# Kernel tuning notes

Measured on AMD Instinct MI355X. Metric: run time of the kernel, lower is better.

## Reference

```python
import jax, jax.numpy as jnp
import numpy as np
from jax import lax

B, C, H, W = 16, 128, 64, 64
S = 16  # d_state


def setup_inputs() -> dict:
    key = jax.random.key(0)
    ks = jax.random.split(key, 12)
    d = {
        'x': jax.random.normal(ks[0], (B, C, H, W), jnp.float32),
        'conv_w': jax.random.normal(ks[1], (C, C, 3, 3), jnp.float32) * (1.0 / np.sqrt(C * 9)),
        'conv_b': jax.random.normal(ks[2], (C,), jnp.float32) * 0.01,
        'dt_w': jax.random.normal(ks[3], (C, C), jnp.float32) * (1.0 / np.sqrt(C)),
        'dt_b': jax.random.normal(ks[4], (C,), jnp.float32) * 0.01,
        'A': jax.random.normal(ks[5], (C, S), jnp.float32),
        'D': jax.random.normal(ks[6], (C,), jnp.float32),
        'g1_w': jax.random.normal(ks[7], (C, C), jnp.float32) * (1.0 / np.sqrt(C)),
        'g1_b': jax.random.normal(ks[8], (C,), jnp.float32) * 0.01,
        'g2_w': jax.random.normal(ks[9], (C, C), jnp.float32) * (1.0 / np.sqrt(C)),
        'g2_b': jax.random.normal(ks[10], (C,), jnp.float32) * 0.01,
    }
    return d


def _forward(x, conv_w, conv_b, dt_w, dt_b, A, D, g1_w, g1_b, g2_w, g2_b):
    identity = x
    # 3x3 conv, padding=1 (SAME)
    x = lax.conv_general_dilated(x, conv_w, (1, 1), 'SAME',
                                 dimension_numbers=('NCHW', 'OIHW', 'NCHW'))
    x = x + conv_b[None, :, None, None]
    # spectral gate: global avg pool -> 1x1 conv -> relu -> 1x1 conv -> sigmoid
    pooled = jnp.mean(x, axis=(2, 3))                       # [B, C]
    g = jax.nn.relu(jnp.einsum('bc,oc->bo', pooled, g1_w) + g1_b)
    g = jax.nn.sigmoid(jnp.einsum('bc,oc->bo', g, g2_w) + g2_b)
    x = x * g[:, :, None, None]
    # ssm scan over H*W tokens
    x_seq = x.transpose(0, 2, 3, 1).reshape(x.shape[0], H * W, C)  # [B, L, C]
    dt = jax.nn.sigmoid(jnp.einsum('blc,oc->blo', x_seq, dt_w) + dt_b)
    An = -jnp.exp(A)   # [C, S]
    Dp = jnp.exp(D)    # [C]

    def step(h, inp):
        xt, dtt = inp  # each [B, C]
        h = h * jnp.exp(An[None] * dtt[:, :, None]) + xt[:, :, None]  # [B, C, S]
        y = jnp.sum(h * An[None], axis=-1) + Dp * xt                   # [B, C]
        return h, y

    h0 = jnp.zeros((x.shape[0], C, S), x.dtype)
    xs = (x_seq.transpose(1, 0, 2), dt.transpose(1, 0, 2))  # [L, B, C]
    _, ys = lax.scan(step, h0, xs)                           # ys: [L, B, C]
    y = ys.transpose(1, 0, 2).reshape(x.shape[0], H, W, C).transpose(0, 3, 1, 2)
    return y + identity


def reference(x, conv_w, conv_b, dt_w, dt_b, A, D, g1_w, g1_b, g2_w, g2_b):
    return _forward(x, conv_w, conv_b, dt_w, dt_b, A, D, g1_w, g1_b, g2_w, g2_b)
```

## Files before the change

### kernel.cpp

```cpp
#include <hip/hip_runtime.h>
#include <hip/hip_bf16.h>
#include <stdint.h>

#define BB 16
#define CC 128
#define HH 64
#define WW 64
#define LL 4096
#define SS 16
#define NCH 64
#define CT 64

typedef __attribute__((ext_vector_type(2))) float f32x2;
typedef __attribute__((ext_vector_type(4))) float f32x4;
typedef __attribute__((ext_vector_type(8))) short short8;
typedef __attribute__((ext_vector_type(4))) unsigned int u32x4;

#define AS1 __attribute__((address_space(1)))
#define AS3 __attribute__((address_space(3)))

__device__ __forceinline__ float bf2f(unsigned short u) {
    union { unsigned int i; float f; } v;
    v.i = ((unsigned int)u) << 16;
    return v.f;
}
__device__ __forceinline__ float asf(unsigned int u) {
    union { unsigned int i; float f; } v;
    v.i = u;
    return v.f;
}
__device__ __forceinline__ unsigned short f2bf(float f) {
    union { float f; unsigned int i; } v;
    v.f = f;
    unsigned int x = v.i;
    return (unsigned short)((x + 0x7fffu + ((x >> 16) & 1u)) >> 16);
}
__device__ __forceinline__ float fexp2(float x) { return __builtin_amdgcn_exp2f(x); }

__global__ __launch_bounds__(256) void k0(const float* __restrict__ x, unsigned short* __restrict__ xT,
                                          const float* __restrict__ conv_w, const float* __restrict__ dt_w,
                                          const float* __restrict__ A, const float* __restrict__ Dv,
                                          const float* __restrict__ g1w, const float* __restrict__ g2w,
                                          short* __restrict__ wf, short* __restrict__ wdtf,
                                          float* __restrict__ An, float* __restrict__ An2, float* __restrict__ Dp,
                                          float* __restrict__ pooled, float* __restrict__ g1wT, float* __restrict__ g2wT) {
    __shared__ float lt[64][65];
    int bid = blockIdx.x;
    int tid = threadIdx.x;
    if (bid < 2048) {
        int b = bid >> 7, rem = bid & 127;
        int tt = rem >> 1, ct = rem & 1;
        int t0 = tt * 64, c0 = ct * 64;
        int colr = tid & 63, rowb = tid >> 6;
#pragma unroll
        for (int r = 0; r < 16; ++r) {
            int row = rowb + r * 4;
            lt[row][colr] = x[(size_t)(b * CC + c0 + row) * LL + t0 + colr];
        }
        __syncthreads();
#pragma unroll
        for (int r = 0; r < 16; ++r) {
            int trow = rowb + r * 4;
            xT[((size_t)b * LL + t0 + trow) * CC + c0 + colr] = f2bf(lt[colr][trow]);
        }
        return;
    }
    int idx = (bid - 2048) * 256 + tid;
    if (idx < 18432) {
        int lane = idx & 63, fr = idx >> 6;
        int nfg = fr & 7, ks = (fr >> 3) & 3, tp = fr >> 5;
        int dy = tp / 3, dx = tp % 3;
        int cout = nfg * 16 + (lane & 15);
        int cin0 = ks * 32 + (lane >> 4) * 8;
        short8 v;
#pragma unroll
        for (int j = 0; j < 8; ++j)
            v[j] = (short)f2bf(conv_w[((cout * CC + cin0 + j) * 3 + dy) * 3 + dx]);
        *(short8*)(wf + (size_t)idx * 8) = v;
    } else if (idx < 20480) {
        int i2 = idx - 18432;
        int lane = i2 & 63, fr = i2 >> 6;
        int nfg = fr & 7, ks = fr >> 3;
        int o = nfg * 16 + (lane & 15);
        int c0 = ks * 32 + (lane >> 4) * 8;
        short8 v;
#pragma unroll
        for (int j = 0; j < 8; ++j) v[j] = (short)f2bf(dt_w[o * CC + c0 + j]);
        *(short8*)(wdtf + (size_t)i2 * 8) = v;
    } else if (idx < 22528) {
        int i3 = idx - 20480;
        float a = -expf(A[i3]);
        An[i3] = a;
        An2[i3] = a * 1.4426950408889634f;
    } else if (idx < 22656) {
        int c = idx - 22528;
        Dp[c] = expf(Dv[c]);
    } else if (idx < 24704) {
        pooled[idx - 22656] = 0.f;
    } else if (idx < 41088) {
        int i = idx - 24704;
        int c = i >> 7, o = i & 127;
        g1wT[i] = g1w[o * 128 + c];
    } else if (idx < 57472) {
        int i = idx - 41088;
        int c = i >> 7, o = i & 127;
        g2wT[i] = g2w[o * 128 + c];
    }
}

__global__ __launch_bounds__(256) void k1(const unsigned short* __restrict__ xT,
                                          const short* __restrict__ wf,
                                          const float* __restrict__ conv_b,
                                          unsigned short* __restrict__ convT,
                                          float* __restrict__ pooled) {
    __shared__ __align__(16) unsigned short slab[3 * 66 * 128];
    int bid = blockIdx.x;
    int b = bid >> 6, h = bid & 63;
    int tid = threadIdx.x;
    int wave = tid >> 6, lane = tid & 63;

    if (tid < 96) {
        int dy = tid >> 5, r = (tid >> 4) & 1, j = tid & 15;
        u32x4 z = {0, 0, 0, 0};
        *(u32x4*)((char*)slab + dy * 16896 + (r ? 16640 : 0) + j * 16) = z;
    }
#pragma unroll
    for (int dy = 0; dy < 3; ++dy) {
        int hs = h + dy - 1;
        char* slabdy = (char*)slab + dy * 16896;
        if (hs >= 0 && hs < HH) {
            const char* src = (const char*)xT + (size_t)(b * LL + hs * 64) * 256;
#pragma unroll
            for (int i = 0; i < 4; ++i) {
                unsigned int Xbase = 256u + (unsigned)i * 4096u + (unsigned)wave * 1024u;
                unsigned int X = Xbase + (unsigned)lane * 16u;
                unsigned int tok = X >> 8;
                unsigned int srcoff = ((X & ~255u) - 256u) | ((X & 255u) ^ ((tok & 7u) << 4));
                __builtin_amdgcn_global_load_lds((const AS1 unsigned int*)(src + srcoff),
                                                 (AS3 unsigned int*)(slabdy + Xbase), 16, 0, 0);
            }
        } else {
            u32x4 z = {0, 0, 0, 0};
#pragma unroll
            for (int i = 0; i < 4; ++i)
                *(u32x4*)(slabdy + 256 + tid * 64 + i * 16) = z;
        }
    }
    __syncthreads();

    int lm = lane & 15, lg = lane >> 4;
    f32x4 acc[4][2];
#pragma unroll
    for (int m = 0; m < 4; ++m)
#pragma unroll
        for (int n = 0; n < 2; ++n) acc[m][n] = (f32x4){0.f, 0.f, 0.f, 0.f};

#pragma unroll
    for (int tp = 0; tp < 9; ++tp) {
        int dy = tp / 3, dx = tp % 3;
        const char* slabdy = (const char*)slab + dy * 16896;
#pragma unroll
        for (int ks = 0; ks < 4; ++ks) {
            short8 bf0 = *(const short8*)(wf + ((size_t)(((tp * 4 + ks) * 8) + wave * 2 + 0) * 64 + lane) * 8);
            short8 bf1 = *(const short8*)(wf + ((size_t)(((tp * 4 + ks) * 8) + wave * 2 + 1) * 64 + lane) * 8);
#pragma unroll
            for (int mf = 0; mf < 4; ++mf) {
                int tok = mf * 16 + lm + dx;
                unsigned int off = (unsigned)((tok * 256 + ks * 64 + lg * 16) ^ ((tok & 7) << 4));
                short8 af = *(const short8*)(slabdy + off);
                acc[mf][0] = __builtin_amdgcn_mfma_f32_16x16x32_bf16(af, bf0, acc[mf][0], 0, 0, 0);
                acc[mf][1] = __builtin_amdgcn_mfma_f32_16x16x32_bf16(af, bf1, acc[mf][1], 0, 0, 0);
            }
        }
    }

    int n0w = wave * 32;
    size_t tokbase = (size_t)(b * LL + h * 64);
    float psum[2] = {0.f, 0.f};
#pragma unroll
    for (int nf = 0; nf < 2; ++nf) {
        int n = n0w + nf * 16 + lm;
        float bias = conv_b[n];
#pragma unroll
        for (int mf = 0; mf < 4; ++mf)
#pragma unroll
            for (int r = 0; r < 4; ++r) {
                int w = mf * 16 + lg * 4 + r;
                float v = acc[mf][nf][r] + bias;
                convT[(tokbase + w) * CC + n] = f2bf(v);
                psum[nf] += v;
            }
    }
#pragma unroll
    for (int nf = 0; nf < 2; ++nf) {
        float s = psum[nf];
        s += __shfl_xor(s, 16);
        s += __shfl_xor(s, 32);
        if (lane < 16) atomicAdd(&pooled[b * CC + n0w + nf * 16 + lane], s);
    }
}

__global__ __launch_bounds__(128) void k2(const float* __restrict__ pooled,
                                          const float* __restrict__ g1wT, const float* __restrict__ g1b,
                                          const float* __restrict__ g2wT, const float* __restrict__ g2b,
                                          float* __restrict__ gate) {
    __shared__ float meanr[128];
    __shared__ float garr[128];
    int b = blockIdx.x;
    int tid = threadIdx.x;
    meanr[tid] = pooled[b * CC + tid] * (1.f / 4096.f);
    __syncthreads();
    float acc = g1b[tid];
    for (int c = 0; c < 128; ++c) acc += meanr[c] * g1wT[c * 128 + tid];
    garr[tid] = fmaxf(acc, 0.f);
    __syncthreads();
    float acc2 = g2b[tid];
    for (int c = 0; c < 128; ++c) acc2 += garr[c] * g2wT[c * 128 + tid];
    gate[b * CC + tid] = __builtin_amdgcn_rcpf(1.f + fexp2(-1.4426950408889634f * acc2));
}

__global__ __launch_bounds__(256) void k3(const unsigned short* __restrict__ convT,
                                          const short* __restrict__ wdtf,
                                          const float* __restrict__ gate,
                                          const float* __restrict__ dt_b,
                                          const float* __restrict__ An2,
                                          unsigned short* __restrict__ dtT,
                                          unsigned int* __restrict__ xdt,
                                          float* __restrict__ hend, float* __restrict__ decay,
                                          int packed) {
    __shared__ __align__(16) unsigned short albuf[64 * 128];
    __shared__ __align__(16) unsigned short dtl[64 * 136];
    __shared__ float gl[128];
    int bid = blockIdx.x;
    int b = bid >> 6, ch = bid & 63, t0 = ch * 64;
    int tid = threadIdx.x;
    int wave = tid >> 6, lane = tid & 63;

    if (tid < 128) gl[tid] = gate[b * CC + tid];
    __syncthreads();

    const char* srcb = (const char*)convT + (size_t)(b * LL + t0) * 256;
#pragma unroll
    for (int i = 0; i < 4; ++i) {
        unsigned int byteoff = (unsigned)((i * 256 + tid) * 16);
        unsigned int tok = byteoff >> 8;
        unsigned int inner = byteoff & 255u;
        int c8 = (int)(inner >> 1);
        short8 v = *(const short8*)(srcb + (size_t)tok * 256 + inner);
#pragma unroll
        for (int j = 0; j < 8; ++j) {
            float f = bf2f((unsigned short)v[j]) * gl[c8 + j];
            v[j] = (short)f2bf(f);
        }
        *(short8*)((char*)albuf + (byteoff ^ ((tok & 7u) << 4))) = v;
    }
    __syncthreads();

    int lm = lane & 15, lg = lane >> 4;
    f32x4 acc[4][2];
#pragma unroll
    for (int m = 0; m < 4; ++m)
#pragma unroll
        for (int n = 0; n < 2; ++n) acc[m][n] = (f32x4){0.f, 0.f, 0.f, 0.f};
#pragma unroll
    for (int ks = 0; ks < 4; ++ks) {
        short8 bf0 = *(const short8*)(wdtf + ((size_t)((ks * 8) + wave * 2 + 0) * 64 + lane) * 8);
        short8 bf1 = *(const short8*)(wdtf + ((size_t)((ks * 8) + wave * 2 + 1) * 64 + lane) * 8);
#pragma unroll
        for (int mf = 0; mf < 4; ++mf) {
            int tok = mf * 16 + lm;
            unsigned int off = (unsigned)((tok * 256 + ks * 64 + lg * 16) ^ ((tok & 7) << 4));
            short8 af = *(const short8*)((const char*)albuf + off);
            acc[mf][0] = __builtin_amdgcn_mfma_f32_16x16x32_bf16(af, bf0, acc[mf][0], 0, 0, 0);
            acc[mf][1] = __builtin_amdgcn_mfma_f32_16x16x32_bf16(af, bf1, acc[mf][1], 0, 0, 0);
        }
    }
#pragma unroll
    for (int nf = 0; nf < 2; ++nf) {
        int o = wave * 32 + nf * 16 + lm;
        float zb = dt_b[o];
#pragma unroll
        for (int mf = 0; mf < 4; ++mf)
#pragma unroll
            for (int r = 0; r < 4; ++r) {
                int tok = mf * 16 + lg * 4 + r;
                float z = acc[mf][nf][r] + zb;
                float d = __builtin_amdgcn_rcpf(1.f + fexp2(-1.4426950408889634f * z));
                unsigned short ub = f2bf(d);
                if (!packed) dtT[(size_t)(b * LL + t0 + tok) * CC + o] = ub;
                dtl[tok * 136 + o] = ub;
            }
    }
    __syncthreads();

    if (packed) {
        int c = tid & 127, tq2 = tid >> 7;
        unsigned int* xdrow = xdt + ((size_t)b * CC + c) * LL + t0 + tq2 * 32;
#pragma unroll
        for (int k = 0; k < 8; ++k) {
            u32x4 w4;
#pragma unroll
            for (int j = 0; j < 4; ++j) {
                int t = tq2 * 32 + k * 4 + j;
                unsigned int xoff = ((unsigned)(t * 256 + c * 2)) ^ (((unsigned)t & 7u) << 4);
                unsigned short xu = *(const unsigned short*)((const char*)albuf + xoff);
                unsigned short du = dtl[t * 136 + c];
                w4[j] = (((unsigned int)du) << 16) | (unsigned int)xu;
            }
            *(u32x4*)(xdrow + k * 4) = w4;
        }
    }

    int c = tid & 127, shalf = tid >> 7, s0 = shalf * 8;
    float a2[8], h[8];
#pragma unroll
    for (int q = 0; q < 2; ++q) {
        f32x4 av = *(const f32x4*)(An2 + c * SS + s0 + q * 4);
#pragma unroll
        for (int j = 0; j < 4; ++j) { a2[q * 4 + j] = av[j]; h[q * 4 + j] = 0.f; }
    }
    float sdt = 0.f;
#pragma unroll 4
    for (int t = 0; t < CT; ++t) {
        unsigned int xoff = ((unsigned)(t * 256 + c * 2)) ^ (((unsigned)t & 7u) << 4);
        float x = bf2f(*(const unsigned short*)((const char*)albuf + xoff));
        float d = bf2f(dtl[t * 136 + c]);
        sdt += d;
#pragma unroll
        for (int s = 0; s < 8; ++s) h[s] = h[s] * fexp2(a2[s] * d) + x;
    }
    size_t base = ((size_t)(b * NCH + ch) * CC + c) * SS + s0;
#pragma unroll
    for (int q = 0; q < 2; ++q) {
        f32x4 hv, dv;
#pragma unroll
        for (int j = 0; j < 4; ++j) {
            hv[j] = h[q * 4 + j];
            dv[j] = fexp2(a2[q * 4 + j] * sdt);
        }
        *(f32x4*)(hend + base + q * 4) = hv;
        *(f32x4*)(decay + base + q * 4) = dv;
    }
}

__global__ __launch_bounds__(256) void k5(const float* __restrict__ hend, const float* __restrict__ decay,
                                          float* __restrict__ H0) {
    int idx = blockIdx.x * 256 + threadIdx.x;
    int b = idx >> 11, rem = idx & 2047;
    size_t base = (size_t)(b * NCH) * 2048 + rem;
    float Hv = 0.f;
    float he = hend[base], de = decay[base];
#pragma unroll 4
    for (int k = 0; k < NCH - 1; ++k) {
        size_t nbase = base + 2048;
        float hn = hend[nbase];
        float dn = decay[nbase];
        H0[base] = Hv;
        Hv = he + Hv * de;
        he = hn; de = dn; base = nbase;
    }
    H0[base] = Hv;
}

__global__ __launch_bounds__(256, 4) void k6p(const unsigned int* __restrict__ xdt,
                                              const float* __restrict__ Antab,
                                              const float* __restrict__ An2tab,
                                              const float* __restrict__ Dp,
                                              const float* __restrict__ H0,
                                              const float* __restrict__ xin,
                                              float* __restrict__ out) {
    __shared__ unsigned short ylds[128][66];
    int bid = blockIdx.x;
    int b = bid >> 6, ch = bid & 63;
    int tid = threadIdx.x;
    int wave = tid >> 6, lane = tid & 63;
    int t0 = ch * CT;
    int c = wave * 32 + (lane & 31);
    int shalf = lane >> 5;
    int s0 = shalf * 8;

    f32x2 a22[4], anv[4], h2[4];
#pragma unroll
    for (int q = 0; q < 2; ++q) {
        f32x4 av = *(const f32x4*)(An2tab + c * SS + s0 + q * 4);
        f32x4 nv = *(const f32x4*)(Antab + c * SS + s0 + q * 4);
        a22[q * 2 + 0] = (f32x2){av[0], av[1]};
        a22[q * 2 + 1] = (f32x2){av[2], av[3]};
        anv[q * 2 + 0] = (f32x2){nv[0], nv[1]};
        anv[q * 2 + 1] = (f32x2){nv[2], nv[3]};
    }
    size_t hbase = ((size_t)(b * NCH + ch) * CC + c) * SS + s0;
#pragma unroll
    for (int q = 0; q < 2; ++q) {
        f32x4 hv = *(const f32x4*)(H0 + hbase + q * 4);
        h2[q * 2 + 0] = (f32x2){hv[0], hv[1]};
        h2[q * 2 + 1] = (f32x2){hv[2], hv[3]};
    }
    float dpc = (shalf == 0) ? Dp[c] : 0.f;
    const u32x4* xdp = (const u32x4*)(xdt + ((size_t)b * CC + c) * LL + t0);

#pragma unroll 4
    for (int t4 = 0; t4 < 16; ++t4) {
        u32x4 w4 = xdp[t4];
#pragma unroll
        for (int j = 0; j < 4; ++j) {
            unsigned int w = w4[j];
            float x = asf(w << 16);
            float d = asf(w & 0xffff0000u);
            f32x2 x2 = {x, x};
            f32x2 d2 = {d, d};
            f32x2 y2 = {0.f, 0.f};
#pragma unroll
            for (int q = 0; q < 4; ++q) {
                f32x2 tq = a22[q] * d2;
                f32x2 e2;
                e2.x = fexp2(tq.x);
                e2.y = fexp2(tq.y);
                h2[q] = h2[q] * e2 + x2;
                y2 += h2[q] * anv[q];
            }
            float yp = y2.x + y2.y + dpc * x;
            float yo = yp + __shfl_xor(yp, 32);
            if (shalf == 0) ylds[c][t4 * 4 + j] = f2bf(yo);
        }
    }
    __syncthreads();

    int tq = tid & 15, rbase = tid >> 4;
#pragma unroll
    for (int k = 0; k < 8; ++k) {
        int row = k * 16 + rbase;
        size_t gi = (size_t)(b * CC + row) * LL + t0 + tq * 4;
        f32x4 xi = *(const f32x4*)(xin + gi);
        f32x4 yo;
#pragma unroll
        for (int j = 0; j < 4; ++j) yo[j] = bf2f(ylds[row][tq * 4 + j]) + xi[j];
        *(f32x4*)(out + gi) = yo;
    }
}

__global__ __launch_bounds__(256, 4) void k6f(const unsigned short* __restrict__ convT,
                                              const unsigned short* __restrict__ dtT,
                                              const float* __restrict__ gate,
                                              const float* __restrict__ Antab,
                                              const float* __restrict__ An2tab,
                                              const float* __restrict__ Dp,
                                              const float* __restrict__ H0,
                                              const float* __restrict__ xin,
                                              float* __restrict__ out) {
    __shared__ unsigned short ylds[128][66];
    int bid = blockIdx.x;
    int b = bid >> 6, ch = bid & 63;
    int tid = threadIdx.x;
    int wave = tid >> 6, lane = tid & 63;
    int t0 = ch * CT;
    int c = wave * 32 + (lane & 31);
    int shalf = lane >> 5;
    int s0 = shalf * 8;

    float a2[8], an[8], h[8];
#pragma unroll
    for (int q = 0; q < 2; ++q) {
        f32x4 av = *(const f32x4*)(An2tab + c * SS + s0 + q * 4);
        f32x4 nv = *(const f32x4*)(Antab + c * SS + s0 + q * 4);
#pragma unroll
        for (int j = 0; j < 4; ++j) { a2[q * 4 + j] = av[j]; an[q * 4 + j] = nv[j]; }
    }
    size_t hbase = ((size_t)(b * NCH + ch) * CC + c) * SS + s0;
#pragma unroll
    for (int q = 0; q < 2; ++q) {
        f32x4 hv = *(const f32x4*)(H0 + hbase + q * 4);
#pragma unroll
        for (int j = 0; j < 4; ++j) h[q * 4 + j] = hv[j];
    }
    float g = gate[b * CC + c];
    float dpc = (shalf == 0) ? Dp[c] : 0.f;
    const unsigned short* xp = convT + (size_t)(b * LL + t0) * CC + c;
    const unsigned short* dp = dtT + (size_t)(b * LL + t0) * CC + c;

#pragma unroll 4
    for (int t = 0; t < CT; ++t) {
        float x = bf2f(xp[t * CC]) * g;
        float d = bf2f(dp[t * CC]);
        float y0 = dpc * x, y1 = 0.f;
#pragma unroll
        for (int s = 0; s < 8; ++s) {
            h[s] = h[s] * fexp2(a2[s] * d) + x;
            if (s & 1) y1 += h[s] * an[s]; else y0 += h[s] * an[s];
        }
        float yp = y0 + y1;
        float yo = yp + __shfl_xor(yp, 32);
        if (shalf == 0) ylds[c][t] = f2bf(yo);
    }
    __syncthreads();

    int tt = tid & 63, wq = tid >> 6;
    size_t outbase = (size_t)b * CC * LL + t0 + tt;
#pragma unroll 4
    for (int rr = 0; rr < 32; ++rr) {
        int row = rr * 4 + wq;
        size_t gi = outbase + (size_t)row * LL;
        out[gi] = bf2f(ylds[row][tt]) + xin[gi];
    }
}

extern "C" void kernel_launch(void* const* d_in, const int* in_sizes, int n_in,
                              void* d_out, int out_size, void* d_ws, size_t ws_size,
                              hipStream_t stream) {
    const float* x      = (const float*)d_in[0];
    const float* conv_w = (const float*)d_in[1];
    const float* conv_b = (const float*)d_in[2];
    const float* dt_w   = (const float*)d_in[3];
    const float* dt_b   = (const float*)d_in[4];
    const float* A      = (const float*)d_in[5];
    const float* D      = (const float*)d_in[6];
    const float* g1w    = (const float*)d_in[7];
    const float* g1b    = (const float*)d_in[8];
    const float* g2w    = (const float*)d_in[9];
    const float* g2b    = (const float*)d_in[10];
    float* outp         = (float*)d_out;
    char* ws = (char*)d_ws;

    const bool P = (ws_size >= 67600896ull);

    unsigned short* xT;
    float *hend, *decay, *H0, *g1wT, *g2wT, *pooled, *gate, *Antab, *An2tab, *Dp;
    unsigned short *convT, *dtT;
    unsigned int* xdt;
    short *wf, *wdtf;

    if (P) {
        xT     = (unsigned short*)(ws + 0);
        hend   = (float*)(ws + 0);
        decay  = (float*)(ws + 8388608);
        convT  = (unsigned short*)(ws + 16777216);
        H0     = (float*)(ws + 16777216);
        xdt    = (unsigned int*)(ws + 33554432);
        dtT    = (unsigned short*)(ws + 33554432);
        wf     = (short*)(ws + 67108864);
        wdtf   = (short*)(ws + 67403776);
        pooled = (float*)(ws + 67436544);
        gate   = (float*)(ws + 67444736);
        Antab  = (float*)(ws + 67452928);
        An2tab = (float*)(ws + 67461120);
        Dp     = (float*)(ws + 67469312);
        g1wT   = (float*)(ws + 67469824);
        g2wT   = (float*)(ws + 67535360);
    } else {
        xT     = (unsigned short*)(ws + 0);
        hend   = (float*)(ws + 0);
        decay  = (float*)(ws + 8388608);
        convT  = (unsigned short*)(ws + 16777216);
        dtT    = (unsigned short*)(ws + 33554432);
        xdt    = (unsigned int*)(ws + 33554432);
        H0     = (float*)(ws + 50331648);
        g1wT   = (float*)(ws + 50331648);
        g2wT   = (float*)(ws + 50397184);
        wf     = (short*)(ws + 58720256);
        wdtf   = (short*)(ws + 59015168);
        pooled = (float*)(ws + 59047936);
        gate   = (float*)(ws + 59056128);
        Antab  = (float*)(ws + 59064320);
        An2tab = (float*)(ws + 59072512);
        Dp     = (float*)(ws + 59080704);
    }

    hipLaunchKernelGGL(k0, dim3(2273), dim3(256), 0, stream, x, xT, conv_w, dt_w, A, D, g1w, g2w,
                       wf, wdtf, Antab, An2tab, Dp, pooled, g1wT, g2wT);
    hipLaunchKernelGGL(k1, dim3(1024), dim3(256), 0, stream, xT, wf, conv_b, convT, pooled);
    hipLaunchKernelGGL(k2, dim3(16), dim3(128), 0, stream, pooled, g1wT, g1b, g2wT, g2b, gate);
    hipLaunchKernelGGL(k3, dim3(1024), dim3(256), 0, stream, convT, wdtf, gate, dt_b, An2tab,
                       dtT, xdt, hend, decay, (int)P);
    hipLaunchKernelGGL(k5, dim3(128), dim3(256), 0, stream, hend, decay, H0);
    if (P) {
        hipLaunchKernelGGL(k6p, dim3(1024), dim3(256), 0, stream, (const unsigned int*)xdt,
                           Antab, An2tab, Dp, H0, x, outp);
    } else {
        hipLaunchKernelGGL(k6f, dim3(1024), dim3(256), 0, stream, convT, dtT, gate,
                           Antab, An2tab, Dp, H0, x, outp);
    }
}
```

Baseline: 126.8 us.

## Split k6p across channel halves with 4 states per lane and quad reductions

The final scan-apply kernel now processes half the channels per block across twice as many blocks. Each lane holds 4 state entries instead of 8, and the per-token output is reduced with two xor shuffles across lane quads. Launch bounds are raised to 6 blocks per CU. The packed writer in k3 is remapped so 16 lanes cover consecutive tokens of one channel, making the global stores more contiguous. The intent is better parallelism and occupancy in the serial scan, at the cost of an extra shuffle per token and more redundant exp work per value loaded.

New measurement: 129.6 us. 1.02x slower.

```diff
diff --git a/kernel.cpp b/kernel.cpp
--- a/kernel.cpp
+++ b/kernel.cpp
@@ -294,20 +294,21 @@
     __syncthreads();
 
     if (packed) {
-        int c = tid & 127, tq2 = tid >> 7;
-        unsigned int* xdrow = xdt + ((size_t)b * CC + c) * LL + t0 + tq2 * 32;
+        int tquad = tid & 15;
+        int cb = tid >> 4;
 #pragma unroll
         for (int k = 0; k < 8; ++k) {
+            int c = k * 16 + cb;
             u32x4 w4;
 #pragma unroll
             for (int j = 0; j < 4; ++j) {
-                int t = tq2 * 32 + k * 4 + j;
+                int t = tquad * 4 + j;
                 unsigned int xoff = ((unsigned)(t * 256 + c * 2)) ^ (((unsigned)t & 7u) << 4);
                 unsigned short xu = *(const unsigned short*)((const char*)albuf + xoff);
                 unsigned short du = dtl[t * 136 + c];
                 w4[j] = (((unsigned int)du) << 16) | (unsigned int)xu;
             }
-            *(u32x4*)(xdrow + k * 4) = w4;
+            *(u32x4*)(xdt + ((size_t)b * CC + c) * LL + t0 + tquad * 4) = w4;
         }
     }
 
@@ -362,41 +363,34 @@
     H0[base] = Hv;
 }
 
-__global__ __launch_bounds__(256, 4) void k6p(const unsigned int* __restrict__ xdt,
+__global__ __launch_bounds__(256, 6) void k6p(const unsigned int* __restrict__ xdt,
                                               const float* __restrict__ Antab,
                                               const float* __restrict__ An2tab,
                                               const float* __restrict__ Dp,
                                               const float* __restrict__ H0,
                                               const float* __restrict__ xin,
                                               float* __restrict__ out) {
-    __shared__ unsigned short ylds[128][66];
+    __shared__ unsigned short ylds[64][66];
     int bid = blockIdx.x;
-    int b = bid >> 6, ch = bid & 63;
+    int b = bid >> 7, rem = bid & 127;
+    int ch = rem >> 1, chalf = rem & 1;
     int tid = threadIdx.x;
     int wave = tid >> 6, lane = tid & 63;
     int t0 = ch * CT;
-    int c = wave * 32 + (lane & 31);
-    int shalf = lane >> 5;
-    int s0 = shalf * 8;
-
-    f32x2 a22[4], anv[4], h2[4];
-#pragma unroll
-    for (int q = 0; q < 2; ++q) {
-        f32x4 av = *(const f32x4*)(An2tab + c * SS + s0 + q * 4);
-        f32x4 nv = *(const f32x4*)(Antab + c * SS + s0 + q * 4);
-        a22[q * 2 + 0] = (f32x2){av[0], av[1]};
-        a22[q * 2 + 1] = (f32x2){av[2], av[3]};
-        anv[q * 2 + 0] = (f32x2){nv[0], nv[1]};
-        anv[q * 2 + 1] = (f32x2){nv[2], nv[3]};
-    }
-    size_t hbase = ((size_t)(b * NCH + ch) * CC + c) * SS + s0;
-#pragma unroll
-    for (int q = 0; q < 2; ++q) {
-        f32x4 hv = *(const f32x4*)(H0 + hbase + q * 4);
-        h2[q * 2 + 0] = (f32x2){hv[0], hv[1]};
-        h2[q * 2 + 1] = (f32x2){hv[2], hv[3]};
-    }
-    float dpc = (shalf == 0) ? Dp[c] : 0.f;
+    int cl = wave * 16 + (lane >> 2);
+    int c = chalf * 64 + cl;
+    int squad = lane & 3;
+    int s0 = squad * 4;
+
+    float a2[4], an[4], h[4];
+    {
+        f32x4 av = *(const f32x4*)(An2tab + c * SS + s0);
+        f32x4 nv = *(const f32x4*)(Antab + c * SS + s0);
+        f32x4 hv = *(const f32x4*)(H0 + ((size_t)(b * NCH + ch) * CC + c) * SS + s0);
+#pragma unroll
+        for (int j = 0; j < 4; ++j) { a2[j] = av[j]; an[j] = nv[j]; h[j] = hv[j]; }
+    }
+    float dpc = (squad == 0) ? Dp[c] : 0.f;
     const u32x4* xdp = (const u32x4*)(xdt + ((size_t)b * CC + c) * LL + t0);
 
 #pragma unroll 4
@@ -407,30 +401,24 @@
             unsigned int w = w4[j];
             float x = asf(w << 16);
             float d = asf(w & 0xffff0000u);
-            f32x2 x2 = {x, x};
-            f32x2 d2 = {d, d};
-            f32x2 y2 = {0.f, 0.f};
+            float y = dpc * x;
 #pragma unroll
             for (int q = 0; q < 4; ++q) {
-                f32x2 tq = a22[q] * d2;
-                f32x2 e2;
-                e2.x = fexp2(tq.x);
-                e2.y = fexp2(tq.y);
-                h2[q] = h2[q] * e2 + x2;
-                y2 += h2[q] * anv[q];
+                h[q] = h[q] * fexp2(a2[q] * d) + x;
+                y += h[q] * an[q];
             }
-            float yp = y2.x + y2.y + dpc * x;
-            float yo = yp + __shfl_xor(yp, 32);
-            if (shalf == 0) ylds[c][t4 * 4 + j] = f2bf(yo);
+            y += __shfl_xor(y, 1);
+            y += __shfl_xor(y, 2);
+            if (squad == 0) ylds[cl][t4 * 4 + j] = f2bf(y);
         }
     }
     __syncthreads();
 
     int tq = tid & 15, rbase = tid >> 4;
 #pragma unroll
-    for (int k = 0; k < 8; ++k) {
+    for (int k = 0; k < 4; ++k) {
         int row = k * 16 + rbase;
-        size_t gi = (size_t)(b * CC + row) * LL + t0 + tq * 4;
+        size_t gi = (size_t)(b * CC + chalf * 64 + row) * LL + t0 + tq * 4;
         f32x4 xi = *(const f32x4*)(xin + gi);
         f32x4 yo;
 #pragma unroll
@@ -573,7 +561,7 @@
                        dtT, xdt, hend, decay, (int)P);
     hipLaunchKernelGGL(k5, dim3(128), dim3(256), 0, stream, hend, decay, H0);
     if (P) {
-        hipLaunchKernelGGL(k6p, dim3(1024), dim3(256), 0, stream, (const unsigned int*)xdt,
+        hipLaunchKernelGGL(k6p, dim3(2048), dim3(256), 0, stream, (const unsigned int*)xdt,
                            Antab, An2tab, Dp, H0, x, outp);
     } else {
         hipLaunchKernelGGL(k6f, dim3(1024), dim3(256), 0, stream, convT, dtT, gate,
```

## Split final scan into half-chunks using mid-chunk states saved by chunk pass

Applied to the files above, without the earlier changes.

The chunk-scan kernel now also saves the state and summed dt at the midpoint of each 64-token chunk. A new final kernel then runs 2048 blocks, each covering 32 tokens, and rebuilds the mid-chunk starting state from H0, the saved midpoint state and its decay. The packed xdt write pattern is also changed to a token-quad-per-thread layout. This halves the serial scan length per block and doubles parallelism, at the cost of extra workspace and extra writes from the chunk kernel. It only runs when the workspace is large enough.

New measurement: 129.3 us. About the same (+2.0%).

```diff
diff --git a/kernel.cpp b/kernel.cpp
--- a/kernel.cpp
+++ b/kernel.cpp
@@ -227,7 +227,8 @@
                                           unsigned short* __restrict__ dtT,
                                           unsigned int* __restrict__ xdt,
                                           float* __restrict__ hend, float* __restrict__ decay,
-                                          int packed) {
+                                          float* __restrict__ hmid, float* __restrict__ sdtmid,
+                                          int packed, int p2) {
     __shared__ __align__(16) unsigned short albuf[64 * 128];
     __shared__ __align__(16) unsigned short dtl[64 * 136];
     __shared__ float gl[128];
@@ -294,32 +295,33 @@
     __syncthreads();
 
     if (packed) {
-        int c = tid & 127, tq2 = tid >> 7;
-        unsigned int* xdrow = xdt + ((size_t)b * CC + c) * LL + t0 + tq2 * 32;
+        int tquad = tid & 15;
+        int cb = tid >> 4;
 #pragma unroll
         for (int k = 0; k < 8; ++k) {
+            int c = k * 16 + cb;
             u32x4 w4;
 #pragma unroll
             for (int j = 0; j < 4; ++j) {
-                int t = tq2 * 32 + k * 4 + j;
+                int t = tquad * 4 + j;
                 unsigned int xoff = ((unsigned)(t * 256 + c * 2)) ^ (((unsigned)t & 7u) << 4);
                 unsigned short xu = *(const unsigned short*)((const char*)albuf + xoff);
                 unsigned short du = dtl[t * 136 + c];
                 w4[j] = (((unsigned int)du) << 16) | (unsigned int)xu;
             }
-            *(u32x4*)(xdrow + k * 4) = w4;
+            *(u32x4*)(xdt + ((size_t)b * CC + c) * LL + t0 + tquad * 4) = w4;
         }
     }
 
     int c = tid & 127, shalf = tid >> 7, s0 = shalf * 8;
-    float a2[8], h[8];
+    float a2[8], h[8], hm[8];
 #pragma unroll
     for (int q = 0; q < 2; ++q) {
         f32x4 av = *(const f32x4*)(An2 + c * SS + s0 + q * 4);
 #pragma unroll
-        for (int j = 0; j < 4; ++j) { a2[q * 4 + j] = av[j]; h[q * 4 + j] = 0.f; }
-    }
-    float sdt = 0.f;
+        for (int j = 0; j < 4; ++j) { a2[q * 4 + j] = av[j]; h[q * 4 + j] = 0.f; hm[q * 4 + j] = 0.f; }
+    }
+    float sdt = 0.f, sdtm = 0.f;
 #pragma unroll 4
     for (int t = 0; t < CT; ++t) {
         unsigned int xoff = ((unsigned)(t * 256 + c * 2)) ^ (((unsigned)t & 7u) << 4);
@@ -328,6 +330,11 @@
         sdt += d;
 #pragma unroll
         for (int s = 0; s < 8; ++s) h[s] = h[s] * fexp2(a2[s] * d) + x;
+        if (t == 31) {
+            sdtm = sdt;
+#pragma unroll
+            for (int s = 0; s < 8; ++s) hm[s] = h[s];
+        }
     }
     size_t base = ((size_t)(b * NCH + ch) * CC + c) * SS + s0;
 #pragma unroll
@@ -340,6 +347,16 @@
         }
         *(f32x4*)(hend + base + q * 4) = hv;
         *(f32x4*)(decay + base + q * 4) = dv;
+    }
+    if (p2) {
+#pragma unroll
+        for (int q = 0; q < 2; ++q) {
+            f32x4 hv;
+#pragma unroll
+            for (int j = 0; j < 4; ++j) hv[j] = hm[q * 4 + j];
+            *(f32x4*)(hmid + base + q * 4) = hv;
+        }
+        if (shalf == 0) sdtmid[(size_t)(b * NCH + ch) * CC + c] = sdtm;
     }
 }
 
@@ -430,6 +447,105 @@
 #pragma unroll
     for (int k = 0; k < 8; ++k) {
         int row = k * 16 + rbase;
+        size_t gi = (size_t)(b * CC + row) * LL + t0 + tq * 4;
+        f32x4 xi = *(const f32x4*)(xin + gi);
+        f32x4 yo;
+#pragma unroll
+        for (int j = 0; j < 4; ++j) yo[j] = bf2f(ylds[row][tq * 4 + j]) + xi[j];
+        *(f32x4*)(out + gi) = yo;
+    }
+}
+
+__global__ __launch_bounds__(256, 4) void k6p2(const unsigned int* __restrict__ xdt,
+                                               const float* __restrict__ Antab,
+                                               const float* __restrict__ An2tab,
+                                               const float* __restrict__ Dp,
+                                               const float* __restrict__ H0,
+                                               const float* __restrict__ hmid,
+                                               const float* __restrict__ sdtmid,
+                                               const float* __restrict__ xin,
+                                               float* __restrict__ out) {
+    __shared__ unsigned short ylds[128][34];
+    int bid = blockIdx.x;
+    int b = bid >> 7, rem = bid & 127;
+    int ch = rem >> 1, half = rem & 1;
+    int tid = threadIdx.x;
+    int wave = tid >> 6, lane = tid & 63;
+    int t0 = ch * CT + half * 32;
+    int c = wave * 32 + (lane & 31);
+    int shalf = lane >> 5;
+    int s0 = shalf * 8;
+
+    f32x2 a22[4], anv[4], h2[4];
+#pragma unroll
+    for (int q = 0; q < 2; ++q) {
+        f32x4 av = *(const f32x4*)(An2tab + c * SS + s0 + q * 4);
+        f32x4 nv = *(const f32x4*)(Antab + c * SS + s0 + q * 4);
+        a22[q * 2 + 0] = (f32x2){av[0], av[1]};
+        a22[q * 2 + 1] = (f32x2){av[2], av[3]};
+        anv[q * 2 + 0] = (f32x2){nv[0], nv[1]};
+        anv[q * 2 + 1] = (f32x2){nv[2], nv[3]};
+    }
+    size_t hbase = ((size_t)(b * NCH + ch) * CC + c) * SS + s0;
+    if (half == 0) {
+#pragma unroll
+        for (int q = 0; q < 2; ++q) {
+            f32x4 hv = *(const f32x4*)(H0 + hbase + q * 4);
+            h2[q * 2 + 0] = (f32x2){hv[0], hv[1]};
+            h2[q * 2 + 1] = (f32x2){hv[2], hv[3]};
+        }
+    } else {
+        float sdtm = sdtmid[(size_t)(b * NCH + ch) * CC + c];
+#pragma unroll
+        for (int q = 0; q < 2; ++q) {
+            f32x4 hv = *(const f32x4*)(H0 + hbase + q * 4);
+            f32x4 hmv = *(const f32x4*)(hmid + hbase + q * 4);
+#pragma unroll
+            for (int j2 = 0; j2 < 2; ++j2) {
+                f32x2 H0v = (j2 == 0) ? (f32x2){hv[0], hv[1]} : (f32x2){hv[2], hv[3]};
+                f32x2 hmv2 = (j2 == 0) ? (f32x2){hmv[0], hmv[1]} : (f32x2){hmv[2], hmv[3]};
+                f32x2 aa = a22[q * 2 + j2];
+                f32x2 e2;
+                e2.x = fexp2(aa.x * sdtm);
+                e2.y = fexp2(aa.y * sdtm);
+                h2[q * 2 + j2] = H0v * e2 + hmv2;
+            }
+        }
+    }
+    float dpc = (shalf == 0) ? Dp[c] : 0.f;
+    const u32x4* xdp = (const u32x4*)(xdt + ((size_t)b * CC + c) * LL + t0);
+
+#pragma unroll 4
+    for (int t4 = 0; t4 < 8; ++t4) {
+        u32x4 w4 = xdp[t4];
+#pragma unroll
+        for (int j = 0; j < 4; ++j) {
+            unsigned int w = w4[j];
+            float x = asf(w << 16);
+            float d = asf(w & 0xffff0000u);
+            f32x2 x2 = {x, x};
+            f32x2 d2 = {d, d};
+            f32x2 y2 = {0.f, 0.f};
+#pragma unroll
+            for (int q = 0; q < 4; ++q) {
+                f32x2 tq = a22[q] * d2;
+                f32x2 e2;
+                e2.x = fexp2(tq.x);
+                e2.y = fexp2(tq.y);
+                h2[q] = h2[q] * e2 + x2;
+                y2 += h2[q] * anv[q];
+            }
+            float yp = y2.x + y2.y + dpc * x;
+            float yo = yp + __shfl_xor(yp, 32);
+            if (shalf == 0) ylds[c][t4 * 4 + j] = f2bf(yo);
+        }
+    }
+    __syncthreads();
+
+    int tq = tid & 7, rbase = tid >> 3;
+#pragma unroll
+    for (int k = 0; k < 4; ++k) {
+        int row = k * 32 + rbase;
         size_t gi = (size_t)(b * CC + row) * LL + t0 + tq * 4;
         f32x4 xi = *(const f32x4*)(xin + gi);
         f32x4 yo;
@@ -521,15 +637,17 @@
     float* outp         = (float*)d_out;
     char* ws = (char*)d_ws;
 
-    const bool P = (ws_size >= 67600896ull);
+    const bool P  = (ws_size >= 67600896ull);
+    const bool P2 = (ws_size >= 76550144ull);
 
     unsigned short* xT;
     float *hend, *decay, *H0, *g1wT, *g2wT, *pooled, *gate, *Antab, *An2tab, *Dp;
+    float *hmid, *sdtmid;
     unsigned short *convT, *dtT;
     unsigned int* xdt;
     short *wf, *wdtf;
 
-    if (P) {
+    if (P2) {
         xT     = (unsigned short*)(ws + 0);
         hend   = (float*)(ws + 0);
         decay  = (float*)(ws + 8388608);
@@ -537,6 +655,27 @@
         H0     = (float*)(ws + 16777216);
         xdt    = (unsigned int*)(ws + 33554432);
         dtT    = (unsigned short*)(ws + 33554432);
+        hmid   = (float*)(ws + 67108864);
+        sdtmid = (float*)(ws + 75497472);
+        wf     = (short*)(ws + 76021760);
+        wdtf   = (short*)(ws + 76316672);
+        pooled = (float*)(ws + 76349440);
+        gate   = (float*)(ws + 76357632);
+        Antab  = (float*)(ws + 76365824);
+        An2tab = (float*)(ws + 76374016);
+        Dp     = (float*)(ws + 76382208);
+        g1wT   = (float*)(ws + 76382720);
+        g2wT   = (float*)(ws + 76448256);
+    } else if (P) {
+        xT     = (unsigned short*)(ws + 0);
+        hend   = (float*)(ws + 0);
+        decay  = (float*)(ws + 8388608);
+        convT  = (unsigned short*)(ws + 16777216);
+        H0     = (float*)(ws + 16777216);
+        xdt    = (unsigned int*)(ws + 33554432);
+        dtT    = (unsigned short*)(ws + 33554432);
+        hmid   = (float*)(ws + 0);
+        sdtmid = (float*)(ws + 0);
         wf     = (short*)(ws + 67108864);
         wdtf   = (short*)(ws + 67403776);
         pooled = (float*)(ws + 67436544);
@@ -553,6 +692,8 @@
         convT  = (unsigned short*)(ws + 16777216);
         dtT    = (unsigned short*)(ws + 33554432);
         xdt    = (unsigned int*)(ws + 33554432);
+        hmid   = (float*)(ws + 0);
+        sdtmid = (float*)(ws + 0);
         H0     = (float*)(ws + 50331648);
         g1wT   = (float*)(ws + 50331648);
         g2wT   = (float*)(ws + 50397184);
@@ -570,9 +711,12 @@
     hipLaunchKernelGGL(k1, dim3(1024), dim3(256), 0, stream, xT, wf, conv_b, convT, pooled);
     hipLaunchKernelGGL(k2, dim3(16), dim3(128), 0, stream, pooled, g1wT, g1b, g2wT, g2b, gate);
     hipLaunchKernelGGL(k3, dim3(1024), dim3(256), 0, stream, convT, wdtf, gate, dt_b, An2tab,
-                       dtT, xdt, hend, decay, (int)P);
+                       dtT, xdt, hend, decay, hmid, sdtmid, (int)P, (int)P2);
     hipLaunchKernelGGL(k5, dim3(128), dim3(256), 0, stream, hend, decay, H0);
-    if (P) {
+    if (P2) {
+        hipLaunchKernelGGL(k6p2, dim3(2048), dim3(256), 0, stream, (const unsigned int*)xdt,
+                           Antab, An2tab, Dp, H0, hmid, sdtmid, x, outp);
+    } else if (P) {
         hipLaunchKernelGGL(k6p, dim3(1024), dim3(256), 0, stream, (const unsigned int*)xdt,
                            Antab, An2tab, Dp, H0, x, outp);
     } else {
```
